# Kernel optimization log

Measured on AMD Instinct MI355X. Metric: run time of the kernel, lower is better.

The kernel has to match this reference:

```python
import jax, jax.numpy as jnp
import numpy as np

B = 1024      # batch
DF = 2048     # dim_feat (hard-coded in module)
DIM = 128     # contrastive feature dim
C = 8192      # class_num
P = 8         # pos_size_per_cls
N = 4         # neg_size_per_cls
BN_EPS = 1e-5


def _l2norm(x, axis):
    n = jnp.sqrt(jnp.sum(x * x, axis=axis, keepdims=True))
    return x / jnp.maximum(n, 1e-12)


def setup_inputs() -> dict:
    key = jax.random.key(0)
    ks = jax.random.split(key, 12)
    inp = {
        'mid_feat_q': jax.random.normal(ks[0], (B, DF), jnp.float32),
        'mid_feat_k': jax.random.normal(ks[1], (B, DF), jnp.float32),
        'labels_q': jax.random.randint(ks[2], (B,), 0, C, jnp.int32),
        'labels_k': jax.random.randint(ks[3], (B,), 0, C, jnp.int32),
        'W1': jax.random.normal(ks[4], (DF, DF), jnp.float32) * 0.02,
        'b1': jnp.zeros((DF,), jnp.float32),
        'gamma': jnp.ones((DF,), jnp.float32),
        'beta': jnp.zeros((DF,), jnp.float32),
        'W2': jax.random.normal(ks[5], (DF, DIM), jnp.float32) * 0.02,
        'b2': jnp.zeros((DIM,), jnp.float32),
        'Wlin': jax.random.normal(ks[6], (DF, C), jnp.float32) * 0.02,
        'blin': jnp.zeros((C,), jnp.float32),
        'neg_queue': _l2norm(jax.random.normal(ks[7], (DIM, N * C), jnp.float32), axis=0),
        'pos_queue': _l2norm(jax.random.normal(ks[8], (DIM, P * C), jnp.float32), axis=0),
        'neg_ptr': jnp.zeros((C,), jnp.int32),
        'pos_ptr': jnp.zeros((C,), jnp.int32),
    }
    return inp


def _mlp(x, W1, b1, gamma, beta, W2, b2):
    # Linear -> BatchNorm1d (training: batch stats, biased var) -> ReLU -> Linear
    h = x @ W1 + b1
    mu = jnp.mean(h, axis=0)
    var = jnp.var(h, axis=0)
    h = (h - mu) * jax.lax.rsqrt(var + BN_EPS) * gamma + beta
    h = jax.nn.relu(h)
    return h @ W2 + b2


def reference(mid_feat_q, mid_feat_k, labels_q, labels_k,
              W1, b1, gamma, beta, W2, b2, Wlin, blin,
              neg_queue, pos_queue, neg_ptr, pos_ptr):
    feat_q = _l2norm(_mlp(mid_feat_q, W1, b1, gamma, beta, W2, b2), axis=1)
    feat_k = _l2norm(_mlp(mid_feat_k, W1, b1, gamma, beta, W2, b2), axis=1)

    # per-sample positive block gather: pos_queue[:, l*P:(l+1)*P]
    posq = pos_queue.reshape(DIM, C, P)          # (dim, C, P)
    pg = posq[:, labels_q, :]                    # (dim, B, P)
    pos_list = jnp.einsum('bd,dbp->bp', feat_q, pg)   # (B, P)

    # negatives: full sim then drop each sample's own-class block of N columns
    full_neg = feat_q @ neg_queue                # (B, N*C)
    cols = jnp.arange(N * (C - 1), dtype=jnp.int32)
    idx = cols[None, :] + N * (cols[None, :] >= labels_q[:, None] * N).astype(jnp.int32)
    neg_list = jnp.take_along_axis(full_neg, idx, axis=1)  # (B, N*(C-1))

    sim_batch = feat_q @ feat_k.T                # (B, B)
    labels_batch = (labels_q[:, None] == labels_k[None, :]).astype(jnp.float32)

    sim_con = jnp.concatenate([sim_batch, pos_list, neg_list], axis=1)
    labels_con = jnp.concatenate(
        [labels_batch, jnp.ones_like(pos_list), jnp.zeros_like(neg_list)], axis=1)

    logit_cls_q = mid_feat_q @ Wlin + blin
    logit_cls_k = mid_feat_k @ Wlin + blin

    # sequential dequeue/enqueue over the key batch (world_size=1 all_gather)
    def step(carry, inp):
        nq, nptr, pq, pptr = carry
        kv, c = inp
        npos = nptr[c]
        nq = nq.at[:, c * N + npos].set(kv)
        nptr = nptr.at[c].set((npos + 1) % N)
        ppos = pptr[c]
        pq = pq.at[:, c * P + ppos].set(kv)
        pptr = pptr.at[c].set((ppos + 1) % P)
        return (nq, nptr, pq, pptr), None

    (neg_queue2, neg_ptr2, pos_queue2, pos_ptr2), _ = jax.lax.scan(
        step, (neg_queue, neg_ptr, pos_queue, pos_ptr),
        (jax.lax.stop_gradient(feat_k), labels_k))

    return (sim_con, labels_con, logit_cls_q, logit_cls_k,
            neg_queue2, pos_queue2, neg_ptr2, pos_ptr2)
```

## Files before the change

### kernel.cpp

```cpp
#include <hip/hip_runtime.h>

typedef unsigned short u16;
typedef __bf16 bf16x8 __attribute__((ext_vector_type(8)));
typedef unsigned short ushort8 __attribute__((ext_vector_type(8)));
typedef float f32x4 __attribute__((ext_vector_type(4)));

typedef const __attribute__((address_space(1))) void gv_t;
typedef __attribute__((address_space(3))) void lv_t;

__device__ __forceinline__ u16 f2bf(float f) {
    union { float f; unsigned u; } x; x.f = f;
    unsigned r = x.u + 0x7fffu + ((x.u >> 16) & 1u);
    return (u16)(r >> 16);
}
__device__ __forceinline__ float bf2f(u16 h) {
    union { unsigned u; float f; } x; x.u = ((unsigned)h) << 16; return x.f;
}
__device__ __forceinline__ bf16x8 as_bf(ushort8 u) {
    union { ushort8 u; bf16x8 b; } x; x.u = u; return x.b;
}

__global__ void k_cast2(const float* __restrict__ in0, const float* __restrict__ in1,
                        u16* __restrict__ out0, u16* __restrict__ out1, long nvec) {
    const float* in = blockIdx.y ? in1 : in0;
    u16* out = blockIdx.y ? out1 : out0;
    long i = (long)blockIdx.x * blockDim.x + threadIdx.x;
    long stride = (long)gridDim.x * blockDim.x;
    for (; i < nvec; i += stride) {
        float4 v = ((const float4*)in)[i];
        u16 o[4] = {f2bf(v.x), f2bf(v.y), f2bf(v.z), f2bf(v.w)};
        *(unsigned long long*)(out + i * 4) = *(unsigned long long*)o;
    }
}

__global__ void k_castT(const float* __restrict__ in, u16* __restrict__ out,
                        int R, int C) {
    __shared__ u16 tile[32][33];
    int c0 = blockIdx.x * 32, r0 = blockIdx.y * 32;
    int tx = threadIdx.x, ty = threadIdx.y;
#pragma unroll
    for (int i = 0; i < 4; i++)
        tile[ty + 8 * i][tx] = f2bf(in[(size_t)(r0 + ty + 8 * i) * C + c0 + tx]);
    __syncthreads();
#pragma unroll
    for (int i = 0; i < 4; i++)
        out[(size_t)(c0 + ty + 8 * i) * R + r0 + tx] = tile[tx][ty + 8 * i];
}

template <int EPI>
__global__ __launch_bounds__(256, 2) void gemm_bt(
    const u16* A0, const u16* A1, const u16* __restrict__ Bt,
    const u16* __restrict__ Bt2, const float* __restrict__ bias,
    const float* __restrict__ bias2, u16* H0, u16* H1, float* C0, float* C1,
    int lda, int ldb, long long ldc, int n_tiles, int Kchunk,
    const int* __restrict__ labels) {
    __shared__ u16 Al[128 * 32];
    __shared__ u16 Bl[128 * 32];

    int bx, by, kc, half;
    if (EPI == 4) {
        int pid = blockIdx.x + blockIdx.y * 8 + blockIdx.z * 640;
        int xcd = pid & 7, idx = pid >> 3;
        by = xcd * 10 + idx % 10;
        int rem = idx / 10;
        bx = rem & 7; half = rem >> 3; kc = 0;
    } else if (EPI == 5) {
        bx = blockIdx.x; by = blockIdx.y; kc = 0; half = 0;
    } else {
        bx = blockIdx.x; by = blockIdx.y % n_tiles; kc = blockIdx.y / n_tiles;
        half = blockIdx.z;
    }
    const u16* A = half ? A1 : A0;

    const u16* B = Bt;
    int bn0 = by * 128;
    if (EPI == 5 && by >= 8) { B = Bt2; bn0 = (by - 8) * 128; }

    const int m0 = bx * 128;
    const int t = threadIdx.x;
    const int w = t >> 6, l = t & 63;
    const int wm = (w & 1) * 64, wn = (w >> 1) * 64;
    const int quad = l >> 4, ln = l & 15;
    const int srow = t >> 2;
    const int sk = (t & 3) * 8;

    f32x4 acc[4][4];
#pragma unroll
    for (int i = 0; i < 4; i++)
#pragma unroll
        for (int j = 0; j < 4; j++) acc[i][j] = f32x4{};

    u16* lAw = Al + (w << 4) * 32;
    u16* lBw = Bl + (w << 4) * 32;

    const int k_begin = kc * Kchunk;
    for (int k0 = k_begin; k0 < k_begin + Kchunk; k0 += 32) {
        if (k0 != k_begin) __syncthreads();
#pragma unroll
        for (int i = 0; i < 2; i++) {
            __builtin_amdgcn_global_load_lds(
                (gv_t*)(A + (size_t)(m0 + srow + i * 64) * lda + k0 + sk),
                (lv_t*)(lAw + i * 64 * 32), 16, 0, 0);
            __builtin_amdgcn_global_load_lds(
                (gv_t*)(B + (size_t)(bn0 + srow + i * 64) * ldb + k0 + sk),
                (lv_t*)(lBw + i * 64 * 32), 16, 0, 0);
        }
        __syncthreads();
        bf16x8 af[4], bb[4];
#pragma unroll
        for (int i = 0; i < 4; i++) {
            af[i] = as_bf(*(const ushort8*)(Al + (wm + i * 16 + ln) * 32 + quad * 8));
            bb[i] = as_bf(*(const ushort8*)(Bl + (wn + i * 16 + ln) * 32 + quad * 8));
        }
#pragma unroll
        for (int i = 0; i < 4; i++)
#pragma unroll
            for (int j = 0; j < 4; j++)
                acc[i][j] = __builtin_amdgcn_mfma_f32_16x16x32_bf16(af[i], bb[j], acc[i][j], 0, 0, 0);
    }

#pragma unroll
    for (int i = 0; i < 4; i++) {
        int row = m0 + wm + i * 16 + quad * 4;
#pragma unroll
        for (int j = 0; j < 4; j++) {
            int cl = wn + j * 16 + ln;
#pragma unroll
            for (int r = 0; r < 4; r++) {
                int rr = row + r;
                float v = acc[i][j][r];
                if (EPI == 2) {
                    int col = by * 128 + cl;
                    float* Cs = half ? C1 : C0;
                    Cs[(size_t)kc * (1024 * (size_t)ldc) + (size_t)rr * ldc + col] = v;
                } else if (EPI == 4) {
                    if (by < 16) {
                        int col = by * 128 + cl;
                        u16* Hs = half ? H1 : H0;
                        Hs[(size_t)rr * 2048 + col] = f2bf(v + bias[col]);
                    } else {
                        int col = (by - 16) * 128 + cl;
                        float* Cs = half ? C1 : C0;
                        Cs[(size_t)rr * 8192 + col] = v + bias2[col];
                    }
                } else if (EPI == 5) {
                    if (by < 8) {
                        int col = by * 128 + cl;
                        C0[(size_t)rr * 33796 + col] = v;
                    } else {
                        int col = (by - 8) * 128 + cl;
                        int L4 = labels[rr] * 4;
                        if (col < L4)
                            C0[(size_t)rr * 33796 + 1032 + col] = v;
                        else if (col >= L4 + 4)
                            C0[(size_t)rr * 33796 + 1032 + col - 4] = v;
                    }
                }
            }
        }
    }
}

__global__ void k_bn_stats(const u16* __restrict__ Hq, const u16* __restrict__ Hk,
                           float* __restrict__ ps, float* __restrict__ ps2) {
    int half = blockIdx.z;
    const u16* H = half ? Hk : Hq;
    int col = blockIdx.x * 256 + threadIdx.x;
    int r0 = blockIdx.y * 64;
    float s = 0.f, s2 = 0.f;
    for (int r = 0; r < 64; r++) {
        float v = bf2f(H[(size_t)(r0 + r) * 2048 + col]);
        s += v; s2 += v * v;
    }
    size_t o = ((size_t)half * 16 + blockIdx.y) * 2048 + col;
    ps[o] = s; ps2[o] = s2;
}

__global__ void k_bn_final(const float* __restrict__ ps, const float* __restrict__ ps2,
                           const float* __restrict__ gamma, const float* __restrict__ beta,
                           float* __restrict__ scale, float* __restrict__ shift) {
    int idx = blockIdx.x * 256 + threadIdx.x;
    int half = idx >> 11, col = idx & 2047;
    float s = 0.f, s2 = 0.f;
    for (int rb = 0; rb < 16; rb++) {
        size_t o = ((size_t)half * 16 + rb) * 2048 + col;
        s += ps[o]; s2 += ps2[o];
    }
    float mu = s * (1.f / 1024.f);
    float var = s2 * (1.f / 1024.f) - mu * mu;
    float sc = gamma[col] * rsqrtf(var + 1e-5f);
    shift[half * 2048 + col] = beta[col] - mu * sc;
    scale[half * 2048 + col] = sc;
}

__global__ void k_bn_apply(u16* Hq, u16* Hk, const float* __restrict__ scale,
                           const float* __restrict__ shift) {
    int row = blockIdx.x, half = blockIdx.y;
    u16* H = half ? Hk : Hq;
    int col = threadIdx.x * 8;
    ushort8 h = *(ushort8*)(H + (size_t)row * 2048 + col);
    ushort8 o;
#pragma unroll
    for (int k = 0; k < 8; k++) {
        float v = bf2f(h[k]) * scale[half * 2048 + col + k] + shift[half * 2048 + col + k];
        o[k] = f2bf(fmaxf(v, 0.f));
    }
    *(ushort8*)(H + (size_t)row * 2048 + col) = o;
}

__global__ void k_l2norm(const float* __restrict__ Fqp, const float* __restrict__ Fkp,
                         const float* __restrict__ b2, float* fqf, float* fkf,
                         u16* fqh, u16* fkh, const float* __restrict__ pq,
                         const int* __restrict__ lq, float* __restrict__ out0) {
    int row = blockIdx.x, half = blockIdx.y, d = threadIdx.x;
    const float* Fp = half ? Fkp : Fqp;
    float x = b2[d];
#pragma unroll
    for (int kc = 0; kc < 8; kc++)
        x += Fp[(size_t)kc * 131072 + (size_t)row * 128 + d];
    float ss = x * x;
#pragma unroll
    for (int off = 32; off >= 1; off >>= 1) ss += __shfl_down(ss, off);
    __shared__ float p[2];
    if ((threadIdx.x & 63) == 0) p[threadIdx.x >> 6] = ss;
    __syncthreads();
    float n = sqrtf(p[0] + p[1]);
    float v = x / fmaxf(n, 1e-12f);
    (half ? fkf : fqf)[(size_t)row * 128 + d] = v;
    (half ? fkh : fqh)[(size_t)row * 128 + d] = f2bf(v);

    if (half == 0) {
        int base = lq[row] * 8;
        const float* pp = pq + (size_t)d * 65536 + base;
        float4 v0 = *(const float4*)pp;
        float4 v1 = *(const float4*)(pp + 4);
        float a[8] = {v * v0.x, v * v0.y, v * v0.z, v * v0.w,
                      v * v1.x, v * v1.y, v * v1.z, v * v1.w};
#pragma unroll
        for (int off = 32; off >= 1; off >>= 1)
#pragma unroll
            for (int q = 0; q < 8; q++) a[q] += __shfl_down(a[q], off);
        __shared__ float pr[2][8];
        if ((threadIdx.x & 63) == 0) {
#pragma unroll
            for (int q = 0; q < 8; q++) pr[threadIdx.x >> 6][q] = a[q];
        }
        __syncthreads();
        if (threadIdx.x < 8)
            out0[(size_t)row * 33796 + 1024 + threadIdx.x] =
                pr[0][threadIdx.x] + pr[1][threadIdx.x];
    }
}

__global__ void k_labels(const int* __restrict__ lq, const int* __restrict__ lk,
                         float* __restrict__ out1) {
    int b = blockIdx.y;
    int j0 = (blockIdx.x * 256 + threadIdx.x) * 8;
    if (j0 >= 33796) return;
    float* o = out1 + (size_t)b * 33796;
    if (j0 >= 1032 && j0 + 8 <= 33796) {
        float4 z = {0.f, 0.f, 0.f, 0.f};
        *(float4*)(o + j0) = z;
        *(float4*)(o + j0 + 4) = z;
    } else {
        int Lq = lq[b];
        for (int k = 0; k < 8 && j0 + k < 33796; k++) {
            int j = j0 + k;
            o[j] = (j < 1024) ? ((Lq == lk[j]) ? 1.f : 0.f) : (j < 1032 ? 1.f : 0.f);
        }
    }
}

__global__ void k_copy2(const float* __restrict__ s1, float* __restrict__ d1, long n1,
                        const float* __restrict__ s2, float* __restrict__ d2, long n2) {
    long i = (long)blockIdx.x * blockDim.x + threadIdx.x;
    long stride = (long)gridDim.x * blockDim.x;
    long tot = n1 + n2;
    for (; i < tot; i += stride) {
        if (i < n1) ((float4*)d1)[i] = ((const float4*)s1)[i];
        else ((float4*)d2)[i - n1] = ((const float4*)s2)[i - n1];
    }
}

__global__ void k_rank(const int* __restrict__ lk, const int* __restrict__ nptr,
                       const int* __restrict__ pptr, int* __restrict__ counts,
                       int* __restrict__ colN, int* __restrict__ colP) {
    __shared__ int lab[1024];
    int tid = threadIdx.x;
    for (int i = tid; i < 1024; i += 128) lab[i] = lk[i];
    __syncthreads();
    int b = blockIdx.x * 128 + tid;
    int c = lab[b];
    int rank = 0, count = 0;
    for (int i = 0; i < 1024; i++) {
        int m = (lab[i] == c);
        count += m;
        rank += (i < b) ? m : 0;
    }
    if (rank == count - 1) counts[c] = count;
    colN[b] = (rank >= count - 4) ? c * 4 + (nptr[c] + rank) % 4 : -1;
    colP[b] = (rank >= count - 8) ? c * 8 + (pptr[c] + rank) % 8 : -1;
}

__global__ void k_scatter_ptrs(const float* __restrict__ fkf,
                               const int* __restrict__ colN, const int* __restrict__ colP,
                               const int* __restrict__ nptr, const int* __restrict__ pptr,
                               const int* __restrict__ counts,
                               float* outN, float* outP, float* outNp, float* outPp) {
    int bid = blockIdx.x;
    if (bid < 512) {
        int b = bid * 2 + (threadIdx.x >> 7);
        int d = threadIdx.x & 127;
        float v = fkf[(size_t)b * 128 + d];
        int cn = colN[b];
        if (cn >= 0) outN[(size_t)d * 32768 + cn] = v;
        int cp = colP[b];
        if (cp >= 0) outP[(size_t)d * 65536 + cp] = v;
    } else {
        int c = (bid - 512) * 256 + threadIdx.x;
        int cnt = counts[c];
        outNp[c] = (float)((nptr[c] + cnt) & 3);
        outPp[c] = (float)((pptr[c] + cnt) & 7);
    }
}

extern "C" void kernel_launch(void* const* d_in, const int* in_sizes, int n_in,
                              void* d_out, int out_size, void* d_ws, size_t ws_size,
                              hipStream_t stream) {
    const float* midq = (const float*)d_in[0];
    const float* midk = (const float*)d_in[1];
    const int* lq     = (const int*)d_in[2];
    const int* lk     = (const int*)d_in[3];
    const float* W1   = (const float*)d_in[4];
    const float* b1   = (const float*)d_in[5];
    const float* gamma= (const float*)d_in[6];
    const float* beta = (const float*)d_in[7];
    const float* W2   = (const float*)d_in[8];
    const float* b2   = (const float*)d_in[9];
    const float* Wlin = (const float*)d_in[10];
    const float* blin = (const float*)d_in[11];
    const float* nq   = (const float*)d_in[12];
    const float* pq   = (const float*)d_in[13];
    const int* nptr   = (const int*)d_in[14];
    const int* pptr   = (const int*)d_in[15];
    (void)in_sizes; (void)n_in; (void)out_size; (void)ws_size;

    float* out = (float*)d_out;
    const size_t O0 = 0;
    const size_t O1 = 34607104;
    const size_t O2 = 69214208;
    const size_t O3 = 77602816;
    const size_t O4 = 85991424;
    const size_t O5 = 90185728;
    const size_t O6 = 98574336;
    const size_t O7 = 98582528;

    char* ws = (char*)d_ws;
    size_t off = 0;
    auto alloc = [&](size_t bytes) -> char* {
        char* p = ws + off;
        off = (off + bytes + 255) & ~(size_t)255;
        return p;
    };
    u16* W1t   = (u16*)alloc((size_t)2048 * 2048 * 2);
    u16* WlinT = (u16*)alloc((size_t)8192 * 2048 * 2);
    u16* W2t   = (u16*)alloc((size_t)128 * 2048 * 2);
    u16* nqT   = (u16*)alloc((size_t)32768 * 128 * 2);
    u16* midqh = (u16*)alloc((size_t)1024 * 2048 * 2);
    u16* midkh = (u16*)alloc((size_t)1024 * 2048 * 2);
    u16* Hq    = (u16*)alloc((size_t)1024 * 2048 * 2);
    u16* Hk    = (u16*)alloc((size_t)1024 * 2048 * 2);
    float* Fq  = (float*)alloc((size_t)8 * 1024 * 128 * 4);
    float* Fk  = (float*)alloc((size_t)8 * 1024 * 128 * 4);
    float* fqf = (float*)alloc((size_t)1024 * 128 * 4);
    float* fkf = (float*)alloc((size_t)1024 * 128 * 4);
    u16* fqh   = (u16*)alloc((size_t)1024 * 128 * 2);
    u16* fkh   = (u16*)alloc((size_t)1024 * 128 * 2);
    float* ps  = (float*)alloc((size_t)2 * 16 * 2048 * 4);
    float* ps2 = (float*)alloc((size_t)2 * 16 * 2048 * 4);
    float* scaleA = (float*)alloc((size_t)2 * 2048 * 4);
    float* shiftA = (float*)alloc((size_t)2 * 2048 * 4);
    int* counts = (int*)alloc(8192 * 4);
    int* colN   = (int*)alloc(1024 * 4);
    int* colP   = (int*)alloc(1024 * 4);

    k_cast2<<<dim3(1024, 2), 256, 0, stream>>>(midq, midk, midqh, midkh,
                                               (long)1024 * 2048 / 4);
    dim3 tb(32, 8);
    k_castT<<<dim3(64, 64), tb, 0, stream>>>(W1, W1t, 2048, 2048);
    k_castT<<<dim3(256, 64), tb, 0, stream>>>(Wlin, WlinT, 2048, 8192);
    k_castT<<<dim3(4, 64), tb, 0, stream>>>(W2, W2t, 2048, 128);
    k_castT<<<dim3(1024, 4), tb, 0, stream>>>(nq, nqT, 128, 32768);

    gemm_bt<4><<<dim3(8, 80, 2), 256, 0, stream>>>(midqh, midkh, W1t, nullptr,
        b1, blin, Hq, Hk, out + O2, out + O3, 2048, 2048, 0, 80, 2048, nullptr);

    k_bn_stats<<<dim3(8, 16, 2), 256, 0, stream>>>(Hq, Hk, ps, ps2);
    k_bn_final<<<16, 256, 0, stream>>>(ps, ps2, gamma, beta, scaleA, shiftA);
    k_bn_apply<<<dim3(1024, 2), 256, 0, stream>>>(Hq, Hk, scaleA, shiftA);

    hipMemsetAsync(counts, 0, 8192 * 4, stream);

    gemm_bt<2><<<dim3(8, 8, 2), 256, 0, stream>>>(Hq, Hk, W2t, nullptr, nullptr,
        nullptr, nullptr, nullptr, Fq, Fk, 2048, 2048, 128, 1, 256, nullptr);

    k_l2norm<<<dim3(1024, 2), 128, 0, stream>>>(Fq, Fk, b2, fqf, fkf, fqh, fkh,
                                                pq, lq, out + O0);

    gemm_bt<5><<<dim3(8, 264, 1), 256, 0, stream>>>(fqh, fqh, fkh, nqT,
        nullptr, nullptr, nullptr, nullptr, out + O0, out + O0,
        128, 128, 33796, 264, 128, lq);

    k_labels<<<dim3(17, 1024), 256, 0, stream>>>(lq, lk, out + O1);

    k_copy2<<<2048, 256, 0, stream>>>(nq, out + O4, 4194304 / 4,
                                      pq, out + O5, 8388608 / 4);

    k_rank<<<8, 128, 0, stream>>>(lk, nptr, pptr, counts, colN, colP);
    k_scatter_ptrs<<<544, 256, 0, stream>>>(fkf, colN, colP, nptr, pptr, counts,
                                            out + O4, out + O5, out + O6, out + O7);
}
```

Baseline: 766.1 us.

## Fuse casts into one prep kernel, BN stats and label writes into GEMM epilogues

The four weight/input cast-transpose launches are merged into a single k_prep kernel. BatchNorm column sums are now accumulated in the first GEMM's epilogue with wave shuffles and atomics, which removes the separate k_bn_stats pass that re-read H. The labels output is written inside the similarity GEMM epilogue and k_l2norm, so the standalone k_labels kernel is dropped. In exchange there are more atomics and extra epilogue stores, and the variance is now computed from fp32 pre-rounding values rather than the bf16 values.

```diff
diff --git a/kernel.cpp b/kernel.cpp
--- a/kernel.cpp
+++ b/kernel.cpp
@@ -20,23 +20,31 @@
     union { ushort8 u; bf16x8 b; } x; x.u = u; return x.b;
 }
 
-__global__ void k_cast2(const float* __restrict__ in0, const float* __restrict__ in1,
-                        u16* __restrict__ out0, u16* __restrict__ out1, long nvec) {
-    const float* in = blockIdx.y ? in1 : in0;
-    u16* out = blockIdx.y ? out1 : out0;
-    long i = (long)blockIdx.x * blockDim.x + threadIdx.x;
-    long stride = (long)gridDim.x * blockDim.x;
-    for (; i < nvec; i += stride) {
+__global__ void k_prep(const float* __restrict__ midq, const float* __restrict__ midk,
+                       u16* __restrict__ midqh, u16* __restrict__ midkh,
+                       const float* __restrict__ W1, u16* __restrict__ W1t,
+                       const float* __restrict__ Wlin, u16* __restrict__ WlinT,
+                       const float* __restrict__ W2, u16* __restrict__ W2t,
+                       const float* __restrict__ nq, u16* __restrict__ nqT) {
+    int bid = blockIdx.x;
+    int t = threadIdx.y * 32 + threadIdx.x;
+    if (bid < 4096) {
+        const float* in = (bid < 2048) ? midq : midk;
+        u16* outp = (bid < 2048) ? midqh : midkh;
+        long i = (long)(bid & 2047) * 256 + t;
         float4 v = ((const float4*)in)[i];
         u16 o[4] = {f2bf(v.x), f2bf(v.y), f2bf(v.z), f2bf(v.w)};
-        *(unsigned long long*)(out + i * 4) = *(unsigned long long*)o;
-    }
-}
-
-__global__ void k_castT(const float* __restrict__ in, u16* __restrict__ out,
-                        int R, int C) {
+        *(unsigned long long*)(outp + i * 4) = *(unsigned long long*)o;
+        return;
+    }
+    int b = bid - 4096;
+    const float* in; u16* outp; int R, C, ctiles;
+    if (b < 4096)       { in = W1;   outp = W1t;   R = 2048; C = 2048;  ctiles = 64; }
+    else if (b < 20480) { b -= 4096;  in = Wlin; outp = WlinT; R = 2048; C = 8192;  ctiles = 256; }
+    else if (b < 20736) { b -= 20480; in = W2;   outp = W2t;   R = 2048; C = 128;   ctiles = 4; }
+    else                { b -= 20736; in = nq;   outp = nqT;   R = 128;  C = 32768; ctiles = 1024; }
+    int c0 = (b % ctiles) * 32, r0 = (b / ctiles) * 32;
     __shared__ u16 tile[32][33];
-    int c0 = blockIdx.x * 32, r0 = blockIdx.y * 32;
     int tx = threadIdx.x, ty = threadIdx.y;
 #pragma unroll
     for (int i = 0; i < 4; i++)
@@ -44,7 +52,7 @@
     __syncthreads();
 #pragma unroll
     for (int i = 0; i < 4; i++)
-        out[(size_t)(c0 + ty + 8 * i) * R + r0 + tx] = tile[tx][ty + 8 * i];
+        outp[(size_t)(c0 + ty + 8 * i) * R + r0 + tx] = tile[tx][ty + 8 * i];
 }
 
 template <int EPI>
@@ -53,7 +61,8 @@
     const u16* __restrict__ Bt2, const float* __restrict__ bias,
     const float* __restrict__ bias2, u16* H0, u16* H1, float* C0, float* C1,
     int lda, int ldb, long long ldc, int n_tiles, int Kchunk,
-    const int* __restrict__ labels) {
+    const int* __restrict__ labels, const int* __restrict__ labelsK,
+    float* outL, float* psA, float* ps2A) {
     __shared__ u16 Al[128 * 32];
     __shared__ u16 Bl[128 * 32];
 
@@ -119,61 +128,96 @@
                 acc[i][j] = __builtin_amdgcn_mfma_f32_16x16x32_bf16(af[i], bb[j], acc[i][j], 0, 0, 0);
     }
 
-#pragma unroll
-    for (int i = 0; i < 4; i++) {
-        int row = m0 + wm + i * 16 + quad * 4;
-#pragma unroll
-        for (int j = 0; j < 4; j++) {
-            int cl = wn + j * 16 + ln;
-#pragma unroll
-            for (int r = 0; r < 4; r++) {
-                int rr = row + r;
-                float v = acc[i][j][r];
-                if (EPI == 2) {
-                    int col = by * 128 + cl;
-                    float* Cs = half ? C1 : C0;
-                    Cs[(size_t)kc * (1024 * (size_t)ldc) + (size_t)rr * ldc + col] = v;
-                } else if (EPI == 4) {
-                    if (by < 16) {
-                        int col = by * 128 + cl;
-                        u16* Hs = half ? H1 : H0;
-                        Hs[(size_t)rr * 2048 + col] = f2bf(v + bias[col]);
-                    } else {
-                        int col = (by - 16) * 128 + cl;
-                        float* Cs = half ? C1 : C0;
-                        Cs[(size_t)rr * 8192 + col] = v + bias2[col];
+    if (EPI == 2) {
+        float* Cs = half ? C1 : C0;
+#pragma unroll
+        for (int i = 0; i < 4; i++) {
+            int row = m0 + wm + i * 16 + quad * 4;
+#pragma unroll
+            for (int j = 0; j < 4; j++) {
+                int col = by * 128 + wn + j * 16 + ln;
+#pragma unroll
+                for (int r = 0; r < 4; r++)
+                    Cs[(size_t)kc * (1024 * (size_t)ldc) + (size_t)(row + r) * ldc + col] = acc[i][j][r];
+            }
+        }
+    } else if (EPI == 4) {
+        if (by < 16) {
+            u16* Hs = half ? H1 : H0;
+            float* psb = psA + half * 2048;
+            float* ps2b = ps2A + half * 2048;
+#pragma unroll
+            for (int j = 0; j < 4; j++) {
+                int col = by * 128 + wn + j * 16 + ln;
+                float bv = bias[col];
+                float sj = 0.f, s2j = 0.f;
+#pragma unroll
+                for (int i = 0; i < 4; i++) {
+                    int row = m0 + wm + i * 16 + quad * 4;
+#pragma unroll
+                    for (int r = 0; r < 4; r++) {
+                        float v = acc[i][j][r] + bv;
+                        Hs[(size_t)(row + r) * 2048 + col] = f2bf(v);
+                        sj += v; s2j += v * v;
                     }
-                } else if (EPI == 5) {
-                    if (by < 8) {
-                        int col = by * 128 + cl;
-                        C0[(size_t)rr * 33796 + col] = v;
-                    } else {
-                        int col = (by - 8) * 128 + cl;
-                        int L4 = labels[rr] * 4;
-                        if (col < L4)
-                            C0[(size_t)rr * 33796 + 1032 + col] = v;
-                        else if (col >= L4 + 4)
-                            C0[(size_t)rr * 33796 + 1032 + col - 4] = v;
+                }
+                sj += __shfl_xor(sj, 16); sj += __shfl_xor(sj, 32);
+                s2j += __shfl_xor(s2j, 16); s2j += __shfl_xor(s2j, 32);
+                if (quad == 0) { atomicAdd(psb + col, sj); atomicAdd(ps2b + col, s2j); }
+            }
+        } else {
+            float* Cs = half ? C1 : C0;
+#pragma unroll
+            for (int j = 0; j < 4; j++) {
+                int col = (by - 16) * 128 + wn + j * 16 + ln;
+                float bv = bias2[col];
+#pragma unroll
+                for (int i = 0; i < 4; i++) {
+                    int row = m0 + wm + i * 16 + quad * 4;
+#pragma unroll
+                    for (int r = 0; r < 4; r++)
+                        Cs[(size_t)(row + r) * 8192 + col] = acc[i][j][r] + bv;
+                }
+            }
+        }
+    } else if (EPI == 5) {
+        if (by < 8) {
+#pragma unroll
+            for (int j = 0; j < 4; j++) {
+                int col = by * 128 + wn + j * 16 + ln;
+                int lblc = labelsK[col];
+#pragma unroll
+                for (int i = 0; i < 4; i++) {
+                    int row = m0 + wm + i * 16 + quad * 4;
+#pragma unroll
+                    for (int r = 0; r < 4; r++) {
+                        int rr = row + r;
+                        C0[(size_t)rr * 33796 + col] = acc[i][j][r];
+                        outL[(size_t)rr * 33796 + col] = (labels[rr] == lblc) ? 1.f : 0.f;
                     }
                 }
             }
-        }
-    }
-}
-
-__global__ void k_bn_stats(const u16* __restrict__ Hq, const u16* __restrict__ Hk,
-                           float* __restrict__ ps, float* __restrict__ ps2) {
-    int half = blockIdx.z;
-    const u16* H = half ? Hk : Hq;
-    int col = blockIdx.x * 256 + threadIdx.x;
-    int r0 = blockIdx.y * 64;
-    float s = 0.f, s2 = 0.f;
-    for (int r = 0; r < 64; r++) {
-        float v = bf2f(H[(size_t)(r0 + r) * 2048 + col]);
-        s += v; s2 += v * v;
-    }
-    size_t o = ((size_t)half * 16 + blockIdx.y) * 2048 + col;
-    ps[o] = s; ps2[o] = s2;
+        } else {
+#pragma unroll
+            for (int j = 0; j < 4; j++) {
+                int col = (by - 8) * 128 + wn + j * 16 + ln;
+#pragma unroll
+                for (int i = 0; i < 4; i++) {
+                    int row = m0 + wm + i * 16 + quad * 4;
+#pragma unroll
+                    for (int r = 0; r < 4; r++) {
+                        int rr = row + r;
+                        int L4 = labels[rr] * 4;
+                        if (col < L4 || col >= L4 + 4) {
+                            size_t dst = (size_t)rr * 33796 + 1032 + col - (col >= L4 + 4 ? 4 : 0);
+                            C0[dst] = acc[i][j][r];
+                            outL[dst] = 0.f;
+                        }
+                    }
+                }
+            }
+        }
+    }
 }
 
 __global__ void k_bn_final(const float* __restrict__ ps, const float* __restrict__ ps2,
@@ -181,11 +225,8 @@
                            float* __restrict__ scale, float* __restrict__ shift) {
     int idx = blockIdx.x * 256 + threadIdx.x;
     int half = idx >> 11, col = idx & 2047;
-    float s = 0.f, s2 = 0.f;
-    for (int rb = 0; rb < 16; rb++) {
-        size_t o = ((size_t)half * 16 + rb) * 2048 + col;
-        s += ps[o]; s2 += ps2[o];
-    }
+    float s = ps[half * 2048 + col];
+    float s2 = ps2[half * 2048 + col];
     float mu = s * (1.f / 1024.f);
     float var = s2 * (1.f / 1024.f) - mu * mu;
     float sc = gamma[col] * rsqrtf(var + 1e-5f);
@@ -211,7 +252,8 @@
 __global__ void k_l2norm(const float* __restrict__ Fqp, const float* __restrict__ Fkp,
                          const float* __restrict__ b2, float* fqf, float* fkf,
                          u16* fqh, u16* fkh, const float* __restrict__ pq,
-                         const int* __restrict__ lq, float* __restrict__ out0) {
+                         const int* __restrict__ lq, float* __restrict__ out0,
+                         float* __restrict__ out1) {
     int row = blockIdx.x, half = blockIdx.y, d = threadIdx.x;
     const float* Fp = half ? Fkp : Fqp;
     float x = b2[d];
@@ -246,27 +288,10 @@
             for (int q = 0; q < 8; q++) pr[threadIdx.x >> 6][q] = a[q];
         }
         __syncthreads();
-        if (threadIdx.x < 8)
+        if (threadIdx.x < 8) {
             out0[(size_t)row * 33796 + 1024 + threadIdx.x] =
                 pr[0][threadIdx.x] + pr[1][threadIdx.x];
-    }
-}
-
-__global__ void k_labels(const int* __restrict__ lq, const int* __restrict__ lk,
-                         float* __restrict__ out1) {
-    int b = blockIdx.y;
-    int j0 = (blockIdx.x * 256 + threadIdx.x) * 8;
-    if (j0 >= 33796) return;
-    float* o = out1 + (size_t)b * 33796;
-    if (j0 >= 1032 && j0 + 8 <= 33796) {
-        float4 z = {0.f, 0.f, 0.f, 0.f};
-        *(float4*)(o + j0) = z;
-        *(float4*)(o + j0 + 4) = z;
-    } else {
-        int Lq = lq[b];
-        for (int k = 0; k < 8 && j0 + k < 33796; k++) {
-            int j = j0 + k;
-            o[j] = (j < 1024) ? ((Lq == lk[j]) ? 1.f : 0.f) : (j < 1032 ? 1.f : 0.f);
+            out1[(size_t)row * 33796 + 1024 + threadIdx.x] = 1.f;
         }
     }
 }
@@ -376,42 +401,37 @@
     float* fkf = (float*)alloc((size_t)1024 * 128 * 4);
     u16* fqh   = (u16*)alloc((size_t)1024 * 128 * 2);
     u16* fkh   = (u16*)alloc((size_t)1024 * 128 * 2);
-    float* ps  = (float*)alloc((size_t)2 * 16 * 2048 * 4);
-    float* ps2 = (float*)alloc((size_t)2 * 16 * 2048 * 4);
+    float* ps  = (float*)alloc((size_t)2 * 2048 * 4);
+    float* ps2 = (float*)alloc((size_t)2 * 2048 * 4);
     float* scaleA = (float*)alloc((size_t)2 * 2048 * 4);
     float* shiftA = (float*)alloc((size_t)2 * 2048 * 4);
     int* counts = (int*)alloc(8192 * 4);
     int* colN   = (int*)alloc(1024 * 4);
     int* colP   = (int*)alloc(1024 * 4);
 
-    k_cast2<<<dim3(1024, 2), 256, 0, stream>>>(midq, midk, midqh, midkh,
-                                               (long)1024 * 2048 / 4);
-    dim3 tb(32, 8);
-    k_castT<<<dim3(64, 64), tb, 0, stream>>>(W1, W1t, 2048, 2048);
-    k_castT<<<dim3(256, 64), tb, 0, stream>>>(Wlin, WlinT, 2048, 8192);
-    k_castT<<<dim3(4, 64), tb, 0, stream>>>(W2, W2t, 2048, 128);
-    k_castT<<<dim3(1024, 4), tb, 0, stream>>>(nq, nqT, 128, 32768);
+    hipMemsetAsync(ps, 0, 2 * 2 * 2048 * 4, stream);
+    hipMemsetAsync(counts, 0, 8192 * 4, stream);
+
+    k_prep<<<28928, dim3(32, 8), 0, stream>>>(midq, midk, midqh, midkh,
+        W1, W1t, Wlin, WlinT, W2, W2t, nq, nqT);
 
     gemm_bt<4><<<dim3(8, 80, 2), 256, 0, stream>>>(midqh, midkh, W1t, nullptr,
-        b1, blin, Hq, Hk, out + O2, out + O3, 2048, 2048, 0, 80, 2048, nullptr);
-
-    k_bn_stats<<<dim3(8, 16, 2), 256, 0, stream>>>(Hq, Hk, ps, ps2);
+        b1, blin, Hq, Hk, out + O2, out + O3, 2048, 2048, 0, 80, 2048,
+        nullptr, nullptr, nullptr, ps, ps2);
+
     k_bn_final<<<16, 256, 0, stream>>>(ps, ps2, gamma, beta, scaleA, shiftA);
     k_bn_apply<<<dim3(1024, 2), 256, 0, stream>>>(Hq, Hk, scaleA, shiftA);
 
-    hipMemsetAsync(counts, 0, 8192 * 4, stream);
-
     gemm_bt<2><<<dim3(8, 8, 2), 256, 0, stream>>>(Hq, Hk, W2t, nullptr, nullptr,
-        nullptr, nullptr, nullptr, Fq, Fk, 2048, 2048, 128, 1, 256, nullptr);
+        nullptr, nullptr, nullptr, Fq, Fk, 2048, 2048, 128, 1, 256,
+        nullptr, nullptr, nullptr, nullptr, nullptr);
 
     k_l2norm<<<dim3(1024, 2), 128, 0, stream>>>(Fq, Fk, b2, fqf, fkf, fqh, fkh,
-                                                pq, lq, out + O0);
+                                                pq, lq, out + O0, out + O1);
 
     gemm_bt<5><<<dim3(8, 264, 1), 256, 0, stream>>>(fqh, fqh, fkh, nqT,
         nullptr, nullptr, nullptr, nullptr, out + O0, out + O0,
-        128, 128, 33796, 264, 128, lq);
-
-    k_labels<<<dim3(17, 1024), 256, 0, stream>>>(lq, lk, out + O1);
+        128, 128, 33796, 264, 128, lq, lk, out + O1, nullptr, nullptr);
 
     k_copy2<<<2048, 256, 0, stream>>>(nq, out + O4, 4194304 / 4,
                                       pq, out + O5, 8388608 / 4);
```

After: 803.0 us. 1.05x slower.
